# Performance work log

Hardware: AMD Instinct MI355X
Metric: run time of the kernel (lower is better)

## Reference

```python
import jax, jax.numpy as jnp
import numpy as np

N_NODES = 20000
N_EDGES = 320000
N_FEAT = 128
MLP_HID = 64
N_GRAPHS = 16
N_LAYERS = 5
EPS = 1e-5


def setup_inputs() -> dict:
    key = jax.random.key(0)
    ks = jax.random.split(key, 8)
    x = jax.random.normal(ks[0], (N_NODES, N_FEAT), dtype=jnp.float32)
    edge_index = jax.random.randint(ks[1], (2, N_EDGES), 0, N_NODES, dtype=jnp.int64)
    batch = jnp.sort(jax.random.randint(ks[2], (N_NODES,), 0, N_GRAPHS, dtype=jnp.int64))
    W1 = jax.random.normal(ks[3], (N_LAYERS, N_FEAT, MLP_HID), dtype=jnp.float32) * 0.05
    b1 = jnp.zeros((N_LAYERS, MLP_HID), dtype=jnp.float32)
    W2 = jax.random.normal(ks[4], (N_LAYERS, MLP_HID, N_FEAT), dtype=jnp.float32) * 0.05
    b2 = jnp.zeros((N_LAYERS, N_FEAT), dtype=jnp.float32)
    gn_weight = jnp.ones((N_LAYERS, N_FEAT), dtype=jnp.float32)
    gn_bias = jnp.zeros((N_LAYERS, N_FEAT), dtype=jnp.float32)
    gn_scale = jnp.ones((N_LAYERS, N_FEAT), dtype=jnp.float32)
    lin_w = jax.random.normal(ks[5], (N_FEAT, 1), dtype=jnp.float32) * 0.05
    lin_b = jnp.zeros((1,), dtype=jnp.float32)
    return {"x": x, "edge_index": edge_index, "batch": batch,
            "W1": W1, "b1": b1, "W2": W2, "b2": b2,
            "gn_weight": gn_weight, "gn_bias": gn_bias, "gn_scale": gn_scale,
            "lin_w": lin_w, "lin_b": lin_b}


def _conv(h, src, dst, W1, b1, W2, b2):
    # message MLP is per-source-node, so compute MLP(x) once per node,
    # then gather by src and scatter-add to dst. Self loops add m[i] at i.
    m = jax.nn.relu(h @ W1 + b1) @ W2 + b2  # [N, C]
    return jax.ops.segment_sum(m[src], dst, num_segments=N_NODES) + m


def _graph_norm(h, batch, cnt, w, b, a):
    mean = jax.ops.segment_sum(h, batch, num_segments=N_GRAPHS) / cnt  # [G, C]
    out = h - a * mean[batch]
    var = jax.ops.segment_sum(out * out, batch, num_segments=N_GRAPHS) / cnt
    out = out * jax.lax.rsqrt(var[batch] + EPS)
    return w * out + b


def reference(x, edge_index, batch, W1, b1, W2, b2, gn_weight, gn_bias, gn_scale, lin_w, lin_b):
    src, dst = edge_index[0], edge_index[1]
    cnt = jax.ops.segment_sum(jnp.ones((N_NODES, 1), x.dtype), batch,
                              num_segments=N_GRAPHS)
    cnt = jnp.maximum(cnt, 1.0)  # [G, 1]
    h = x
    for i in range(N_LAYERS):
        g = _conv(h, src, dst, W1[i], b1[i], W2[i], b2[i])
        g = _graph_norm(g, batch, cnt, gn_weight[i], gn_bias[i], gn_scale[i])
        g = jax.nn.relu(g)  # dropout is identity in eval mode
        h = g if i == 0 else g + h  # residual from layer 2 onward
    pooled = jax.ops.segment_sum(h, batch, num_segments=N_GRAPHS) / cnt  # [G, C]
    return pooled @ lin_w + lin_b  # [G, 1]
```

## Files before the change

kernel.cpp:

```cpp
#include <hip/hip_runtime.h>

#define N_NODES 20000
#define N_EDGES 320000
#define N_FEAT 128
#define MLP_HID 64
#define N_GRAPHS 16
#define N_LAYERS 5
#define EPS 1e-5f

typedef __attribute__((ext_vector_type(8))) short short8;
typedef __attribute__((ext_vector_type(4))) float f32x4;

__device__ inline float bf2f(unsigned short u) { return __uint_as_float(((unsigned)u) << 16); }
__device__ inline unsigned short f2bf(float f) {
  unsigned u = __float_as_uint(f);
  u += 0x7FFF + ((u >> 16) & 1);
  return (unsigned short)(u >> 16);
}


__global__ __launch_bounds__(256) void k_prep(const float* __restrict__ W1, const float* __restrict__ W2,
                                              unsigned short* __restrict__ w1t, unsigned short* __restrict__ w2t,
                                              int* __restrict__ deg) {
  int idx = blockIdx.x * 256 + threadIdx.x;
  if (idx < N_NODES) deg[idx] = 0;
  if (idx < 40960) {
    int l = idx >> 13, rem = idx & 8191;
    int n = rem >> 7, k = rem & 127;
    w1t[idx] = f2bf(W1[l * 8192 + k * 64 + n]);
  } else {
    int j = idx - 40960;
    int l = j >> 13, rem = j & 8191;
    int n = rem >> 6, k = rem & 63;
    w2t[j] = f2bf(W2[l * 8192 + k * 128 + n]);
  }
}


__global__ __launch_bounds__(256) void k_deg(const int* __restrict__ dst, int* __restrict__ deg) {
  int e = blockIdx.x * 256 + threadIdx.x;
  atomicAdd(&deg[dst[e]], 1);
}

__global__ __launch_bounds__(1024) void k_scan(const int* __restrict__ deg, int* __restrict__ rowptr,
                                               int* __restrict__ cursor, const int* __restrict__ batch,
                                               float* __restrict__ cntf, float* __restrict__ pooled) {
  __shared__ int sdata[1024];
  __shared__ int spos[17];
  constexpr int CH = 20;
  int t = threadIdx.x;
  for (int i = t; i < N_GRAPHS * N_FEAT; i += 1024) pooled[i] = 0.0f;
  int base = t * CH;
  int loc[CH];
  int partial = 0;
#pragma unroll
  for (int i = 0; i < CH; i++) {
    int idx = base + i;
    int v = (idx < N_NODES) ? deg[idx] : 0;
    loc[i] = v;
    partial += v;
  }
  sdata[t] = partial;
  __syncthreads();
  for (int off = 1; off < 1024; off <<= 1) {
    int v = (t >= off) ? sdata[t - off] : 0;
    __syncthreads();
    sdata[t] += v;
    __syncthreads();
  }
  int run = sdata[t] - partial;
#pragma unroll
  for (int i = 0; i < CH; i++) {
    int idx = base + i;
    if (idx < N_NODES) {
      rowptr[idx] = run;
      cursor[idx] = run;
      run += loc[i];
    }
  }
  if (t == 1023) rowptr[N_NODES] = sdata[1023];
  if (t < 17) {
    int lo = 0, hi = N_NODES;
    while (lo < hi) {
      int mid = (lo + hi) >> 1;
      if (batch[mid] < t) lo = mid + 1; else hi = mid;
    }
    spos[t] = lo;
  }
  __syncthreads();
  if (t < N_GRAPHS) cntf[t] = fmaxf((float)(spos[t + 1] - spos[t]), 1.0f);
}

__global__ __launch_bounds__(256) void k_fill(const int* __restrict__ src, const int* __restrict__ dst,
                                              int* __restrict__ cursor, unsigned short* __restrict__ src_sorted) {
  int e = blockIdx.x * 256 + threadIdx.x;
  int d = dst[e];
  int p = atomicAdd(&cursor[d], 1);
  src_sorted[p] = (unsigned short)src[e];
}


#define PADK 136
#define PADH 72

__global__ __launch_bounds__(256) void k_mlp(const float* __restrict__ hinf,
                                             const unsigned short* __restrict__ hinb, int fp32in,
                                             unsigned short* __restrict__ mout,
                                             const unsigned short* __restrict__ w1t,
                                             const unsigned short* __restrict__ w2t,
                                             const float* __restrict__ b1, const float* __restrict__ b2) {
  __shared__ __align__(16) short hS[64 * PADK];
  __shared__ __align__(16) short w1S[64 * PADK];
  __shared__ __align__(16) short hidS[64 * PADH];
  __shared__ __align__(16) short w2S[128 * PADH];
  __shared__ float b1S[64];
  __shared__ float b2S[128];
  int t = threadIdx.x;
  int r0 = blockIdx.x * 64;
  if (fp32in) {
#pragma unroll
    for (int i = 0; i < 8; i++) {
      int idx = t + i * 256;
      int row = idx >> 5, c4 = idx & 31;
      float4 v = (r0 + row < N_NODES) ? ((const float4*)hinf)[(size_t)(r0 + row) * 32 + c4]
                                      : make_float4(0.f, 0.f, 0.f, 0.f);
      ushort4 s;
      s.x = f2bf(v.x); s.y = f2bf(v.y); s.z = f2bf(v.z); s.w = f2bf(v.w);
      *(ushort4*)&hS[row * PADK + c4 * 4] = s;
    }
  } else {
#pragma unroll
    for (int i = 0; i < 4; i++) {
      int idx = t + i * 256;
      int row = idx >> 4, c8 = idx & 15;
      int4 v = (r0 + row < N_NODES) ? ((const int4*)hinb)[(size_t)(r0 + row) * 16 + c8]
                                    : make_int4(0, 0, 0, 0);
      *(int4*)&hS[row * PADK + c8 * 8] = v;
    }
  }
#pragma unroll
  for (int i = 0; i < 4; i++) {
    int idx = t + i * 256;
    *(int4*)&w1S[(idx >> 4) * PADK + (idx & 15) * 8] = ((const int4*)w1t)[idx];
    *(int4*)&w2S[(idx >> 3) * PADH + (idx & 7) * 8] = ((const int4*)w2t)[idx];
  }
  if (t < 64) b1S[t] = b1[t];
  else if (t < 192) b2S[t - 64] = b2[t - 64];
  __syncthreads();

  int w = t >> 6, lane = t & 63, lm = lane & 15, quad = lane >> 4;
  int mrow = w * 16 + lm;
  int orow = w * 16 + quad * 4;

  f32x4 zero = {0.f, 0.f, 0.f, 0.f};
  f32x4 acc[4] = {zero, zero, zero, zero};
#pragma unroll
  for (int k0 = 0; k0 < 128; k0 += 32) {
    short8 a = *(const short8*)&hS[mrow * PADK + k0 + quad * 8];
#pragma unroll
    for (int nt = 0; nt < 4; nt++) {
      short8 b = *(const short8*)&w1S[(nt * 16 + lm) * PADK + k0 + quad * 8];
      acc[nt] = __builtin_amdgcn_mfma_f32_16x16x32_bf16(a, b, acc[nt], 0, 0, 0);
    }
  }
#pragma unroll
  for (int nt = 0; nt < 4; nt++) {
    int col = nt * 16 + lm;
    float bb = b1S[col];
#pragma unroll
    for (int r = 0; r < 4; r++)
      hidS[(orow + r) * PADH + col] = (short)f2bf(fmaxf(acc[nt][r] + bb, 0.0f));
  }
  __syncthreads();

  f32x4 acc2[8] = {zero, zero, zero, zero, zero, zero, zero, zero};
#pragma unroll
  for (int k0 = 0; k0 < 64; k0 += 32) {
    short8 a = *(const short8*)&hidS[mrow * PADH + k0 + quad * 8];
#pragma unroll
    for (int nt = 0; nt < 8; nt++) {
      short8 b = *(const short8*)&w2S[(nt * 16 + lm) * PADH + k0 + quad * 8];
      acc2[nt] = __builtin_amdgcn_mfma_f32_16x16x32_bf16(a, b, acc2[nt], 0, 0, 0);
    }
  }
#pragma unroll
  for (int nt = 0; nt < 8; nt++) {
    int col = nt * 16 + lm;
    float bb = b2S[col];
#pragma unroll
    for (int r = 0; r < 4; r++)
      hS[(orow + r) * PADK + col] = (short)f2bf(acc2[nt][r] + bb);
  }
  __syncthreads();
#pragma unroll
  for (int i = 0; i < 4; i++) {
    int idx = t + i * 256;
    int row = idx >> 4, cc = idx & 15;
    if (r0 + row < N_NODES)
      ((int4*)mout)[(size_t)(r0 + row) * 16 + cc] = *(const int4*)&hS[row * PADK + cc * 8];
  }
}


__global__ __launch_bounds__(256) void k_scatter(const unsigned short* __restrict__ mbf,
                                                 unsigned short* __restrict__ g,
                                                 const int* __restrict__ rowptr,
                                                 const unsigned short* __restrict__ srcs,
                                                 float* __restrict__ s1, float* __restrict__ s2) {
  if (blockIdx.x == 0) {
    for (int i = threadIdx.x; i < N_GRAPHS * N_FEAT; i += 256) { s1[i] = 0.0f; s2[i] = 0.0f; }
  }
  int node = (blockIdx.x * 256 + threadIdx.x) >> 6;
  int lane = threadIdx.x & 63;
  int quarter = lane >> 4;
  int q16 = lane & 15;
  const float4* m4 = (const float4*)mbf;
  float acc[8];
  union BU { float4 f; unsigned short u[8]; };
  if (quarter == 0) {
    BU U; U.f = m4[(size_t)node * 16 + q16];
#pragma unroll
    for (int j = 0; j < 8; j++) acc[j] = bf2f(U.u[j]);
  } else {
#pragma unroll
    for (int j = 0; j < 8; j++) acc[j] = 0.0f;
  }
  int e = rowptr[node], e1 = rowptr[node + 1];
  for (; e + 16 <= e1; e += 16) {
    int i0 = srcs[e + quarter];
    int i1 = srcs[e + 4 + quarter];
    int i2 = srcs[e + 8 + quarter];
    int i3 = srcs[e + 12 + quarter];
    BU U0, U1, U2, U3;
    U0.f = m4[(size_t)i0 * 16 + q16];
    U1.f = m4[(size_t)i1 * 16 + q16];
    U2.f = m4[(size_t)i2 * 16 + q16];
    U3.f = m4[(size_t)i3 * 16 + q16];
#pragma unroll
    for (int j = 0; j < 8; j++)
      acc[j] += (bf2f(U0.u[j]) + bf2f(U1.u[j])) + (bf2f(U2.u[j]) + bf2f(U3.u[j]));
  }
  for (; e + 4 <= e1; e += 4) {
    BU U0; U0.f = m4[(size_t)srcs[e + quarter] * 16 + q16];
#pragma unroll
    for (int j = 0; j < 8; j++) acc[j] += bf2f(U0.u[j]);
  }
  if (e + quarter < e1) {
    BU U0; U0.f = m4[(size_t)srcs[e + quarter] * 16 + q16];
#pragma unroll
    for (int j = 0; j < 8; j++) acc[j] += bf2f(U0.u[j]);
  }
#pragma unroll
  for (int j = 0; j < 8; j++) {
    acc[j] += __shfl_xor(acc[j], 16);
    acc[j] += __shfl_xor(acc[j], 32);
  }
  if (quarter == 0) {
    union { int4 i4; unsigned short u[8]; } P;
#pragma unroll
    for (int j = 0; j < 8; j++) P.u[j] = f2bf(acc[j]);
    ((int4*)g)[(size_t)node * 16 + q16] = P.i4;
  }
}


#define STAT_CHUNK 8

__global__ __launch_bounds__(128) void k_stats(const unsigned short* __restrict__ in,
                                               const int* __restrict__ batch,
                                               float* __restrict__ s1, float* __restrict__ s2) {
  int n0 = blockIdx.x * STAT_CHUNK;
  int c = threadIdx.x;
  int curg = batch[n0];
  float a1 = 0.0f, a2 = 0.0f;
#pragma unroll
  for (int k = 0; k < STAT_CHUNK; k++) {
    int n = n0 + k;
    int gg = batch[n];
    if (gg != curg) {
      atomicAdd(&s1[curg * 128 + c], a1);
      atomicAdd(&s2[curg * 128 + c], a2);
      a1 = 0.0f; a2 = 0.0f;
      curg = gg;
    }
    float v = bf2f(in[(size_t)n * 128 + c]);
    a1 += v;
    a2 += v * v;
  }
  atomicAdd(&s1[curg * 128 + c], a1);
  atomicAdd(&s2[curg * 128 + c], a2);
}


__global__ __launch_bounds__(256) void k_apply(const unsigned short* __restrict__ gin,
                                               unsigned short* __restrict__ h,
                                               const int* __restrict__ batch,
                                               const float* __restrict__ s1, const float* __restrict__ s2,
                                               const float* __restrict__ cntf,
                                               const float* __restrict__ w, const float* __restrict__ b,
                                               const float* __restrict__ a, int residual) {
  int idx = blockIdx.x * 256 + threadIdx.x;
  int n = idx >> 5, c4 = idx & 31;
  int gg = batch[n];
  float invc = 1.0f / cntf[gg];
  float4 sm = ((const float4*)s1)[gg * 32 + c4];
  float4 se = ((const float4*)s2)[gg * 32 + c4];
  float4 av = ((const float4*)a)[c4];
  float4 wv = ((const float4*)w)[c4];
  float4 bv = ((const float4*)b)[c4];
  ushort4 gu = ((const ushort4*)gin)[idx];
  float4 gv = make_float4(bf2f(gu.x), bf2f(gu.y), bf2f(gu.z), bf2f(gu.w));
  float4 hv = make_float4(0.f, 0.f, 0.f, 0.f);
  if (residual) {
    ushort4 hu = ((const ushort4*)h)[idx];
    hv = make_float4(bf2f(hu.x), bf2f(hu.y), bf2f(hu.z), bf2f(hu.w));
  }
  float4 o;
#define APPLY1(X)                                                          \
  {                                                                        \
    float mean = sm.X * invc;                                              \
    float ex2 = se.X * invc;                                               \
    float ac = av.X;                                                       \
    float var = fmaxf(ex2 - mean * mean * (2.0f * ac - ac * ac), 0.0f);    \
    float d = gv.X - ac * mean;                                            \
    float y = wv.X * (d * rsqrtf(var + EPS)) + bv.X;                       \
    y = fmaxf(y, 0.0f);                                                    \
    o.X = residual ? (y + hv.X) : y;                                       \
  }
  APPLY1(x) APPLY1(y) APPLY1(z) APPLY1(w)
#undef APPLY1
  ushort4 ou;
  ou.x = f2bf(o.x); ou.y = f2bf(o.y); ou.z = f2bf(o.z); ou.w = f2bf(o.w);
  ((ushort4*)h)[idx] = ou;
}


__global__ __launch_bounds__(256) void k_apply_pool(const unsigned short* __restrict__ gin,
                                                    const unsigned short* __restrict__ h,
                                                    const int* __restrict__ batch,
                                                    const float* __restrict__ s1, const float* __restrict__ s2,
                                                    const float* __restrict__ cntf,
                                                    const float* __restrict__ gw, const float* __restrict__ gb,
                                                    const float* __restrict__ ga,
                                                    float* __restrict__ pooled) {
  __shared__ float pS[8][128];
  int t = threadIdx.x;
  int idx = blockIdx.x * 256 + t;
  int n = idx >> 5, c4 = idx & 31;
  int gg = batch[n];
  float invc = 1.0f / cntf[gg];
  float4 sm = ((const float4*)s1)[gg * 32 + c4];
  float4 se = ((const float4*)s2)[gg * 32 + c4];
  float4 av = ((const float4*)ga)[c4];
  float4 wv = ((const float4*)gw)[c4];
  float4 bv = ((const float4*)gb)[c4];
  ushort4 gu = ((const ushort4*)gin)[idx];
  float4 gv = make_float4(bf2f(gu.x), bf2f(gu.y), bf2f(gu.z), bf2f(gu.w));
  ushort4 hu = ((const ushort4*)h)[idx];
  float4 hv = make_float4(bf2f(hu.x), bf2f(hu.y), bf2f(hu.z), bf2f(hu.w));
  float4 o;
#define APPLY1(X)                                                          \
  {                                                                        \
    float mean = sm.X * invc;                                              \
    float ex2 = se.X * invc;                                               \
    float ac = av.X;                                                       \
    float var = fmaxf(ex2 - mean * mean * (2.0f * ac - ac * ac), 0.0f);    \
    float d = gv.X - ac * mean;                                            \
    float y = wv.X * (d * rsqrtf(var + EPS)) + bv.X;                       \
    y = fmaxf(y, 0.0f);                                                    \
    o.X = y + hv.X;                                                        \
  }
  APPLY1(x) APPLY1(y) APPLY1(z) APPLY1(w)
#undef APPLY1
  *(float4*)&pS[t >> 5][c4 * 4] = o;
  __syncthreads();
  int n0 = blockIdx.x * 8;
  int gA = batch[n0], gB = batch[n0 + 7];
  if (t < 128) {
    if (gA == gB) {
      float s = 0.f;
#pragma unroll
      for (int ww = 0; ww < 8; ww++) s += pS[ww][t];
      atomicAdd(&pooled[gA * 128 + t], s);
    } else {
#pragma unroll
      for (int ww = 0; ww < 8; ww++) atomicAdd(&pooled[batch[n0 + ww] * 128 + t], pS[ww][t]);
    }
  }
}


__global__ __launch_bounds__(256) void k_final(const float* __restrict__ pooled, const float* __restrict__ cntf,
                                               const float* __restrict__ lw, const float* __restrict__ lb,
                                               float* __restrict__ out) {
  int lane = threadIdx.x & 63, wave = threadIdx.x >> 6;
  for (int gi = 0; gi < 4; gi++) {
    int gidx = wave * 4 + gi;
    float s = pooled[gidx * 128 + lane] * lw[lane] + pooled[gidx * 128 + 64 + lane] * lw[64 + lane];
    for (int o = 32; o >= 1; o >>= 1) s += __shfl_down(s, o);
    if (lane == 0) out[gidx] = s / cntf[gidx] + lb[0];
  }
}


extern "C" void kernel_launch(void* const* d_in, const int* in_sizes, int n_in,
                              void* d_out, int out_size, void* d_ws, size_t ws_size,
                              hipStream_t stream) {
  const float* x = (const float*)d_in[0];
  const int* ei = (const int*)d_in[1];
  const int* batch = (const int*)d_in[2];
  const float* W1 = (const float*)d_in[3];
  const float* b1 = (const float*)d_in[4];
  const float* W2 = (const float*)d_in[5];
  const float* b2 = (const float*)d_in[6];
  const float* gnw = (const float*)d_in[7];
  const float* gnb = (const float*)d_in[8];
  const float* gna = (const float*)d_in[9];
  const float* lw = (const float*)d_in[10];
  const float* lb = (const float*)d_in[11];
  float* out = (float*)d_out;

  const int* srcI = ei;
  const int* dstI = ei + N_EDGES;

  char* p = (char*)d_ws;
  unsigned short* hbuf = (unsigned short*)(p + 0);
  unsigned short* mbuf = (unsigned short*)(p + 10240000);
  unsigned short* gbuf = (unsigned short*)(p + 20480000);
  unsigned short* src_sorted = (unsigned short*)(p + 30720000);
  int* rowptr = (int*)(p + 32000000);
  int* cursor = (int*)(p + 32080128);
  int* deg = (int*)(p + 32160256);
  float* cntf = (float*)(p + 32240512);
  float* s1buf = (float*)(p + 32240640);
  float* s2buf = (float*)(p + 32248832);
  float* pooled = (float*)(p + 32257024);
  unsigned short* w1t = (unsigned short*)(p + 32265216);
  unsigned short* w2t = (unsigned short*)(p + 32347136);

  k_prep<<<320, 256, 0, stream>>>(W1, W2, w1t, w2t, deg);
  k_deg<<<N_EDGES / 256, 256, 0, stream>>>(dstI, deg);
  k_scan<<<1, 1024, 0, stream>>>(deg, rowptr, cursor, batch, cntf, pooled);
  k_fill<<<N_EDGES / 256, 256, 0, stream>>>(srcI, dstI, cursor, src_sorted);

  for (int i = 0; i < N_LAYERS; i++) {
    k_mlp<<<(N_NODES + 63) / 64, 256, 0, stream>>>(x, hbuf, i == 0 ? 1 : 0, mbuf,
                                                   w1t + (size_t)i * 8192, w2t + (size_t)i * 8192,
                                                   b1 + (size_t)i * 64, b2 + (size_t)i * 128);
    k_scatter<<<N_NODES / 4, 256, 0, stream>>>(mbuf, gbuf, rowptr, src_sorted, s1buf, s2buf);
    k_stats<<<N_NODES / STAT_CHUNK, 128, 0, stream>>>(gbuf, batch, s1buf, s2buf);
    if (i < N_LAYERS - 1) {
      k_apply<<<N_NODES * N_FEAT / 4 / 256, 256, 0, stream>>>(gbuf, hbuf, batch, s1buf, s2buf, cntf,
                                                              gnw + (size_t)i * 128, gnb + (size_t)i * 128,
                                                              gna + (size_t)i * 128, i > 0 ? 1 : 0);
    } else {
      k_apply_pool<<<N_NODES / 8, 256, 0, stream>>>(gbuf, hbuf, batch, s1buf, s2buf, cntf,
                                                    gnw + (size_t)i * 128, gnb + (size_t)i * 128,
                                                    gna + (size_t)i * 128, pooled);
    }
  }

  k_final<<<1, 256, 0, stream>>>(pooled, cntf, lw, lb, out);
}
```

Before: 331.7 us.

## Split message buffer into feature halves and gather each half in separate passes

```diff
diff --git a/kernel.cpp b/kernel.cpp
--- a/kernel.cpp
+++ b/kernel.cpp
@@ -7,6 +7,7 @@
 #define N_GRAPHS 16
 #define N_LAYERS 5
 #define EPS 1e-5f
+#define NCHUNK 5000
 
 typedef __attribute__((ext_vector_type(8))) short short8;
 typedef __attribute__((ext_vector_type(4))) float f32x4;
@@ -105,7 +106,8 @@
 
 __global__ __launch_bounds__(256) void k_mlp(const float* __restrict__ hinf,
                                              const unsigned short* __restrict__ hinb, int fp32in,
-                                             unsigned short* __restrict__ mout,
+                                             unsigned short* __restrict__ mlo,
+                                             unsigned short* __restrict__ mhi,
                                              const unsigned short* __restrict__ w1t,
                                              const unsigned short* __restrict__ w2t,
                                              const float* __restrict__ b1, const float* __restrict__ b2) {
@@ -196,13 +198,17 @@
   for (int i = 0; i < 4; i++) {
     int idx = t + i * 256;
     int row = idx >> 4, cc = idx & 15;
-    if (r0 + row < N_NODES)
-      ((int4*)mout)[(size_t)(r0 + row) * 16 + cc] = *(const int4*)&hS[row * PADK + cc * 8];
-  }
-}
-
-
-__global__ __launch_bounds__(256) void k_scatter(const unsigned short* __restrict__ mbf,
+    if (r0 + row < N_NODES) {
+      int4 v = *(const int4*)&hS[row * PADK + cc * 8];
+      if (cc < 8) ((int4*)mlo)[(size_t)(r0 + row) * 8 + cc] = v;
+      else        ((int4*)mhi)[(size_t)(r0 + row) * 8 + (cc - 8)] = v;
+    }
+  }
+}
+
+
+__global__ __launch_bounds__(256) void k_scatter(const unsigned short* __restrict__ mlo,
+                                                 const unsigned short* __restrict__ mhi,
                                                  unsigned short* __restrict__ g,
                                                  const int* __restrict__ rowptr,
                                                  const unsigned short* __restrict__ srcs,
@@ -210,56 +216,50 @@
   if (blockIdx.x == 0) {
     for (int i = threadIdx.x; i < N_GRAPHS * N_FEAT; i += 256) { s1[i] = 0.0f; s2[i] = 0.0f; }
   }
-  int node = (blockIdx.x * 256 + threadIdx.x) >> 6;
-  int lane = threadIdx.x & 63;
-  int quarter = lane >> 4;
-  int q16 = lane & 15;
-  const float4* m4 = (const float4*)mbf;
+  int pass = blockIdx.x / NCHUNK;
+  int chunk = blockIdx.x - pass * NCHUNK;
+  int t = threadIdx.x;
+  int node = chunk * 4 + (t >> 6);
+  int lane = t & 63;
+  int egrp = lane >> 3;
+  int c8 = lane & 7;
+  const float4* m4 = (const float4*)(pass ? mhi : mlo);
   float acc[8];
   union BU { float4 f; unsigned short u[8]; };
-  if (quarter == 0) {
-    BU U; U.f = m4[(size_t)node * 16 + q16];
+  if (egrp == 0) {
+    BU U; U.f = m4[(size_t)node * 8 + c8];
 #pragma unroll
     for (int j = 0; j < 8; j++) acc[j] = bf2f(U.u[j]);
   } else {
 #pragma unroll
     for (int j = 0; j < 8; j++) acc[j] = 0.0f;
   }
-  int e = rowptr[node], e1 = rowptr[node + 1];
-  for (; e + 16 <= e1; e += 16) {
-    int i0 = srcs[e + quarter];
-    int i1 = srcs[e + 4 + quarter];
-    int i2 = srcs[e + 8 + quarter];
-    int i3 = srcs[e + 12 + quarter];
-    BU U0, U1, U2, U3;
-    U0.f = m4[(size_t)i0 * 16 + q16];
-    U1.f = m4[(size_t)i1 * 16 + q16];
-    U2.f = m4[(size_t)i2 * 16 + q16];
-    U3.f = m4[(size_t)i3 * 16 + q16];
-#pragma unroll
-    for (int j = 0; j < 8; j++)
-      acc[j] += (bf2f(U0.u[j]) + bf2f(U1.u[j])) + (bf2f(U2.u[j]) + bf2f(U3.u[j]));
-  }
-  for (; e + 4 <= e1; e += 4) {
-    BU U0; U0.f = m4[(size_t)srcs[e + quarter] * 16 + q16];
+  int e = rowptr[node] + egrp, e1 = rowptr[node + 1];
+  for (; e + 8 < e1; e += 16) {
+    int i0 = srcs[e];
+    int i1 = srcs[e + 8];
+    BU U0, U1;
+    U0.f = m4[(size_t)i0 * 8 + c8];
+    U1.f = m4[(size_t)i1 * 8 + c8];
+#pragma unroll
+    for (int j = 0; j < 8; j++) acc[j] += bf2f(U0.u[j]) + bf2f(U1.u[j]);
+  }
+  if (e < e1) {
+    BU U0; U0.f = m4[(size_t)srcs[e] * 8 + c8];
 #pragma unroll
     for (int j = 0; j < 8; j++) acc[j] += bf2f(U0.u[j]);
   }
-  if (e + quarter < e1) {
-    BU U0; U0.f = m4[(size_t)srcs[e + quarter] * 16 + q16];
-#pragma unroll
-    for (int j = 0; j < 8; j++) acc[j] += bf2f(U0.u[j]);
-  }
 #pragma unroll
   for (int j = 0; j < 8; j++) {
+    acc[j] += __shfl_xor(acc[j], 8);
     acc[j] += __shfl_xor(acc[j], 16);
     acc[j] += __shfl_xor(acc[j], 32);
   }
-  if (quarter == 0) {
+  if (egrp == 0) {
     union { int4 i4; unsigned short u[8]; } P;
 #pragma unroll
     for (int j = 0; j < 8; j++) P.u[j] = f2bf(acc[j]);
-    ((int4*)g)[(size_t)node * 16 + q16] = P.i4;
+    ((int4*)g)[(size_t)node * 16 + pass * 8 + c8] = P.i4;
   }
 }
 
@@ -425,7 +425,8 @@
 
   char* p = (char*)d_ws;
   unsigned short* hbuf = (unsigned short*)(p + 0);
-  unsigned short* mbuf = (unsigned short*)(p + 10240000);
+  unsigned short* mlo = (unsigned short*)(p + 10240000);
+  unsigned short* mhi = (unsigned short*)(p + 12800000);
   unsigned short* gbuf = (unsigned short*)(p + 20480000);
   unsigned short* src_sorted = (unsigned short*)(p + 30720000);
   int* rowptr = (int*)(p + 32000000);
@@ -444,10 +445,10 @@
   k_fill<<<N_EDGES / 256, 256, 0, stream>>>(srcI, dstI, cursor, src_sorted);
 
   for (int i = 0; i < N_LAYERS; i++) {
-    k_mlp<<<(N_NODES + 63) / 64, 256, 0, stream>>>(x, hbuf, i == 0 ? 1 : 0, mbuf,
+    k_mlp<<<(N_NODES + 63) / 64, 256, 0, stream>>>(x, hbuf, i == 0 ? 1 : 0, mlo, mhi,
                                                    w1t + (size_t)i * 8192, w2t + (size_t)i * 8192,
                                                    b1 + (size_t)i * 64, b2 + (size_t)i * 128);
-    k_scatter<<<N_NODES / 4, 256, 0, stream>>>(mbuf, gbuf, rowptr, src_sorted, s1buf, s2buf);
+    k_scatter<<<2 * NCHUNK, 256, 0, stream>>>(mlo, mhi, gbuf, rowptr, src_sorted, s1buf, s2buf);
     k_stats<<<N_NODES / STAT_CHUNK, 128, 0, stream>>>(gbuf, batch, s1buf, s2buf);
     if (i < N_LAYERS - 1) {
       k_apply<<<N_NODES * N_FEAT / 4 / 256, 256, 0, stream>>>(gbuf, hbuf, batch, s1buf, s2buf, cntf,
```

Result: slower. 352.0 us (+6.1%).
